# Optimization experiments

Measured on AMD Instinct MI355X. Metric: run time of the kernel, lower is better.

The kernel has to match this reference:

```python
import jax, jax.numpy as jnp
import numpy as np

N, D, H = 50000, 128, 2        # nodes, hidden_size(=ffn_size=out_channels), heads
E = 800000                      # edges
C = D                           # per-head out_channels (PyG TransformerConv)
EPS = 1e-5

def layer_norm(x, g, b):
    mu = jnp.mean(x, axis=-1, keepdims=True)
    var = jnp.mean((x - mu) ** 2, axis=-1, keepdims=True)
    return (x - mu) / jnp.sqrt(var + EPS) * g + b

def setup_inputs() -> dict:
    key = jax.random.key(0)
    ks = jax.random.split(key, 16)
    s_in = 1.0 / np.sqrt(D)
    s_ffn = 1.0 / np.sqrt(D)
    return {
        "x": jax.random.normal(ks[0], (N, D), jnp.float32),
        "edge_index": jax.random.randint(ks[1], (2, E), 0, N, jnp.int64),
        "ln1_g": jnp.ones((D,), jnp.float32),
        "ln1_b": jnp.zeros((D,), jnp.float32),
        "Wq": jax.random.normal(ks[2], (D, H * C), jnp.float32) * s_in,
        "bq": jnp.zeros((H * C,), jnp.float32),
        "Wk": jax.random.normal(ks[3], (D, H * C), jnp.float32) * s_in,
        "bk": jnp.zeros((H * C,), jnp.float32),
        "Wv": jax.random.normal(ks[4], (D, H * C), jnp.float32) * s_in,
        "bv": jnp.zeros((H * C,), jnp.float32),
        "Wskip": jax.random.normal(ks[5], (D, C), jnp.float32) * s_in,
        "bskip": jnp.zeros((C,), jnp.float32),
        "ln2_g": jnp.ones((D,), jnp.float32),
        "ln2_b": jnp.zeros((D,), jnp.float32),
        "W1": jax.random.normal(ks[6], (D, D), jnp.float32) * s_ffn,
        "b1": jnp.zeros((D,), jnp.float32),
        "W2": jax.random.normal(ks[7], (D, D), jnp.float32) * s_ffn,
        "b2": jnp.zeros((D,), jnp.float32),
    }

def reference(x, edge_index, ln1_g, ln1_b, Wq, bq, Wk, bk, Wv, bv,
              Wskip, bskip, ln2_g, ln2_b, W1, b1, W2, b2):
    src, dst = edge_index[0], edge_index[1]  # messages flow src(j) -> dst(i)
    n = x.shape[0]

    # --- self-attention block (pre-norm) ---
    y = layer_norm(x, ln1_g, ln1_b)
    q = (y @ Wq + bq).reshape(n, H, C)
    k = (y @ Wk + bk).reshape(n, H, C)
    v = (y @ Wv + bv).reshape(n, H, C)

    # per-edge attention logits [E, H]
    alpha = jnp.einsum('ehc,ehc->eh', q[dst], k[src]) / jnp.sqrt(jnp.float32(C))
    # softmax over incoming edges of each dst node
    m = jax.ops.segment_max(alpha, dst, num_segments=n)          # [N, H]
    p = jnp.exp(alpha - m[dst])                                  # [E, H]
    denom = jax.ops.segment_sum(p, dst, num_segments=n)          # [N, H]
    a = p / denom[dst]                                           # [E, H]

    attn = jax.ops.segment_sum(a[:, :, None] * v[src], dst, num_segments=n)  # [N,H,C]
    out = attn.mean(axis=1) + (y @ Wskip + bskip)  # concat=False mean + root skip
    x = x + out  # residual (dropout is identity at eval)

    # --- FFN block (pre-norm) ---
    h = layer_norm(x, ln2_g, ln2_b)
    h = jax.nn.gelu(h @ W1 + b1, approximate=False) @ W2 + b2
    return x + h
```

## Files before the change

### kernel.cpp

```cpp
#include <hip/hip_runtime.h>
#include <hip/hip_bf16.h>
#include <math.h>


typedef unsigned short u16;
using short8 = __attribute__((ext_vector_type(8))) short;
using f32x4  = __attribute__((ext_vector_type(4))) float;
using f32x2  = __attribute__((ext_vector_type(2))) float;
using u32x4  = __attribute__((ext_vector_type(4))) unsigned int;

#define EST 64

__device__ __forceinline__ float bf2f(u16 u) {
    return __uint_as_float(((unsigned int)u) << 16);
}
__device__ __forceinline__ u16 f2bf(float f) {
    __hip_bfloat16 h = __float2bfloat16(f);
    return __builtin_bit_cast(u16, h);
}
__device__ __forceinline__ float bfe(short8 v, int j) {
    return bf2f((u16)v[j]);
}
__device__ __forceinline__ void fp8x4_to_f32(int w, float* out) {
    f32x2 lo = __builtin_amdgcn_cvt_pk_f32_fp8(w, false);
    f32x2 hi = __builtin_amdgcn_cvt_pk_f32_fp8(w, true);
    out[0] = lo[0]; out[1] = lo[1]; out[2] = hi[0]; out[3] = hi[1];
}
__device__ __forceinline__ unsigned pack_fp8x4(float4 f) {
    unsigned w = 0;
    w = (unsigned)__builtin_amdgcn_cvt_pk_fp8_f32(f.x, f.y, (int)w, false);
    w = (unsigned)__builtin_amdgcn_cvt_pk_fp8_f32(f.z, f.w, (int)w, true);
    return w;
}

__global__ __launch_bounds__(256) void fused_prep_ln(
    const float* __restrict__ x, const float* __restrict__ ln1g,
    const float* __restrict__ ln1b,
    const float* __restrict__ Wq, const float* __restrict__ Wk,
    const float* __restrict__ Wv, const float* __restrict__ Ws,
    const float* __restrict__ W1, const float* __restrict__ W2,
    const float* __restrict__ bq, const float* __restrict__ bk,
    const float* __restrict__ bv, const float* __restrict__ bs,
    u16* __restrict__ wt, float* __restrict__ bc,
    u16* __restrict__ y, int* __restrict__ cnt, int n,
    const int* __restrict__ edst, const int* __restrict__ esrcIn,
    int* __restrict__ ebuk, int e, int histBlocks)
{
    if (blockIdx.x < (unsigned)histBlocks) {
        int stride = histBlocks * 256;
        for (int i = blockIdx.x * 256 + threadIdx.x; i < e; i += stride) {
            int d = edst[i];
            int r = atomicAdd(&cnt[d], 1);
            if (r < EST) ebuk[(size_t)d * EST + r] = esrcIn[i];
        }
        return;
    }
    int gsz = (gridDim.x - histBlocks) * 256;
    int gtid = (blockIdx.x - histBlocks) * 256 + threadIdx.x;

    for (int i = gtid; i < 147456 + 896; i += gsz) {
        if (i < 147456) {
            const float* W; int N; int base;
            if      (i <  32768) { W = Wq; N = 256; base = 0; }
            else if (i <  65536) { W = Wk; N = 256; base = 32768; }
            else if (i <  98304) { W = Wv; N = 256; base = 65536; }
            else if (i < 114688) { W = Ws; N = 128; base = 98304; }
            else if (i < 131072) { W = W1; N = 128; base = 114688; }
            else                 { W = W2; N = 128; base = 131072; }
            int j = i - base;
            int nIdx = j >> 7, k = j & 127;
            wt[i] = f2bf(W[(size_t)k * N + nIdx]);
        } else {
            int j = i - 147456;
            float v;
            if      (j < 256) v = bq[j];
            else if (j < 512) v = bk[j - 256];
            else if (j < 768) v = bv[j - 512];
            else              v = bs[j - 768];
            bc[j] = v;
        }
    }
    int lane = threadIdx.x & 63;
    int gw = gtid >> 6, nw = gsz >> 6;
    for (int row = gw; row < n; row += nw) {
        size_t base = (size_t)row * 128;
        float v0 = x[base + lane];
        float v1 = x[base + 64 + lane];
        float s1 = v0 + v1, s2 = v0 * v0 + v1 * v1;
        for (int o = 1; o <= 32; o <<= 1) {
            s1 += __shfl_xor(s1, o);
            s2 += __shfl_xor(s2, o);
        }
        float mu = s1 * (1.f / 128.f);
        float var = s2 * (1.f / 128.f) - mu * mu;
        float rstd = rsqrtf(var + 1e-5f);
        y[base + lane]      = f2bf((v0 - mu) * rstd * ln1g[lane] + ln1b[lane]);
        y[base + 64 + lane] = f2bf((v1 - mu) * rstd * ln1g[64 + lane] + ln1b[64 + lane]);
    }
}

__global__ __launch_bounds__(256, 6) void qkv_gemm(
    const u16* __restrict__ A, const u16* __restrict__ Bt,
    const float* __restrict__ bias, u16* __restrict__ qbuf,
    unsigned char* __restrict__ kv,
    float* __restrict__ skip, int n)
{
    __shared__ float epi[4][32 * 33];
    int bid = blockIdx.x;
    int wc = threadIdx.x >> 6, lane = threadIdx.x & 63;
    int r0 = bid * 32;
    int lm = lane & 15, quad = lane >> 4;

    int ar0 = r0 + lm;       if (ar0 > n - 1) ar0 = n - 1;
    int ar1 = r0 + 16 + lm;  if (ar1 > n - 1) ar1 = n - 1;
    const u16* aB0 = A + (size_t)ar0 * 128 + quad * 8;
    const u16* aB1 = A + (size_t)ar1 * 128 + quad * 8;
    short8 a0_0 = *(const short8*)(aB0 + 0);
    short8 a0_1 = *(const short8*)(aB0 + 32);
    short8 a0_2 = *(const short8*)(aB0 + 64);
    short8 a0_3 = *(const short8*)(aB0 + 96);
    short8 a1_0 = *(const short8*)(aB1 + 0);
    short8 a1_1 = *(const short8*)(aB1 + 32);
    short8 a1_2 = *(const short8*)(aB1 + 64);
    short8 a1_3 = *(const short8*)(aB1 + 96);
    asm volatile("" : "+v"(a0_0), "+v"(a0_1), "+v"(a0_2), "+v"(a0_3),
                      "+v"(a1_0), "+v"(a1_1), "+v"(a1_2), "+v"(a1_3));

    int rr = lane & 31, hh = lane >> 5;
    int row = r0 + rr;
    bool rowOk = row < n;
    float* ep = epi[wc];

    for (int by = 0; by < 7; ++by) {
        int c0 = by * 128;
        const u16* bBase = Bt + (size_t)(c0 + wc * 32 + lm) * 128 + quad * 8;
        f32x4 acc[2][2] = {};
#pragma unroll
        for (int kx = 0; kx < 4; ++kx) {
            short8 a0 = (kx == 0) ? a0_0 : (kx == 1) ? a0_1 : (kx == 2) ? a0_2 : a0_3;
            short8 a1 = (kx == 0) ? a1_0 : (kx == 1) ? a1_1 : (kx == 2) ? a1_2 : a1_3;
#pragma unroll
            for (int j = 0; j < 2; ++j) {
                short8 bj = *(const short8*)(bBase + (size_t)j * 16 * 128 + kx * 32);
                acc[0][j] = __builtin_amdgcn_mfma_f32_16x16x32_bf16(a0, bj, acc[0][j], 0, 0, 0);
                acc[1][j] = __builtin_amdgcn_mfma_f32_16x16x32_bf16(a1, bj, acc[1][j], 0, 0, 0);
            }
        }
#pragma unroll
        for (int j = 0; j < 2; ++j) {
            float bv = bias[c0 + wc * 32 + j * 16 + lm];
#pragma unroll
            for (int rt = 0; rt < 2; ++rt)
#pragma unroll
                for (int i2 = 0; i2 < 4; ++i2)
                    ep[(rt * 16 + quad * 4 + i2) * 33 + j * 16 + lm]
                        = acc[rt][j][i2] + bv;
        }
        if (rowOk) {
            const float* ws = ep + rr * 33 + hh * 16;
            int colW = wc * 32 + hh * 16;
            if (c0 < 256) {
                u16* dp = qbuf + (size_t)row * 256 + c0 + colW;
                short8 o0, o1;
#pragma unroll
                for (int jj = 0; jj < 8; ++jj) {
                    o0[jj] = (short)f2bf(ws[jj]);
                    o1[jj] = (short)f2bf(ws[8 + jj]);
                }
                *(short8*)(dp + 0) = o0;
                *(short8*)(dp + 8) = o1;
            } else if (c0 < 512) {
                int kc = (c0 - 256) + colW;
                int h = kc >> 7, c = kc & 127;
                unsigned char* kb = kv + (size_t)row * 512 + h * 256 + (c >> 3) * 16;
                uint2 o0, o1;
                o0.x = pack_fp8x4(make_float4(ws[0],  ws[1],  ws[2],  ws[3]));
                o0.y = pack_fp8x4(make_float4(ws[4],  ws[5],  ws[6],  ws[7]));
                o1.x = pack_fp8x4(make_float4(ws[8],  ws[9],  ws[10], ws[11]));
                o1.y = pack_fp8x4(make_float4(ws[12], ws[13], ws[14], ws[15]));
                *(uint2*)kb = o0;
                *(uint2*)(kb + 16) = o1;
            } else if (c0 < 768) {
                int vc = (c0 - 512) + colW;
                int h = vc >> 7, c = vc & 127;
                unsigned char* vb = kv + (size_t)row * 512 + h * 256 + (c >> 3) * 16 + 8;
                uint2 o0, o1;
                o0.x = pack_fp8x4(make_float4(ws[0],  ws[1],  ws[2],  ws[3]));
                o0.y = pack_fp8x4(make_float4(ws[4],  ws[5],  ws[6],  ws[7]));
                o1.x = pack_fp8x4(make_float4(ws[8],  ws[9],  ws[10], ws[11]));
                o1.y = pack_fp8x4(make_float4(ws[12], ws[13], ws[14], ws[15]));
                *(uint2*)vb = o0;
                *(uint2*)(vb + 16) = o1;
            } else {
                float* dp = skip + (size_t)row * 128 + colW;
#pragma unroll
                for (int m2 = 0; m2 < 4; ++m2)
                    *(float4*)(dp + m2 * 4) = *(const float4*)(ws + m2 * 4);
            }
        }
    }
}

__global__ __launch_bounds__(256) void attn_kernel(
    const u16* __restrict__ qbuf, const unsigned char* __restrict__ kv,
    const int* __restrict__ cnt,
    const int* __restrict__ ebuk, const float* __restrict__ x,
    float* __restrict__ sx, const float* __restrict__ g2,
    const float* __restrict__ b2, u16* __restrict__ y, int n, int nwaves)
{
    int wid = threadIdx.x >> 6, lane = threadIdx.x & 63;
    int gw = blockIdx.x * 4 + wid;
    int slot = lane >> 5;
    int sub  = lane & 15;
    int head = (lane >> 4) & 1;
    int colOff = head * 128 + sub * 8;
    int kvOff  = head * 256 + sub * 16;
    const float scale = 0.08838834764831845f;

    for (int i = gw; i < n; i += nwaves) {
        short8 q8 = *(const short8*)(qbuf + (size_t)i * 256 + colOff);
        float qf[8];
#pragma unroll
        for (int j = 0; j < 8; ++j) qf[j] = bfe(q8, j) * scale;

        int deg = cnt[i]; if (deg > EST) deg = EST;
        int beg = i * EST, end = beg + deg;
        float l = 0.f;
        float acc[8] = {};

        int t = beg + slot;
        for (; t + 14 < end; t += 16) {
            int ss[8];
#pragma unroll
            for (int m = 0; m < 8; ++m) ss[m] = ebuk[t + 2 * m];
            u32x4 k0 = *(const u32x4*)(kv + (size_t)ss[0] * 512 + kvOff);
            u32x4 k1 = *(const u32x4*)(kv + (size_t)ss[1] * 512 + kvOff);
            u32x4 k2 = *(const u32x4*)(kv + (size_t)ss[2] * 512 + kvOff);
            u32x4 k3 = *(const u32x4*)(kv + (size_t)ss[3] * 512 + kvOff);
            u32x4 k4 = *(const u32x4*)(kv + (size_t)ss[4] * 512 + kvOff);
            u32x4 k5 = *(const u32x4*)(kv + (size_t)ss[5] * 512 + kvOff);
            u32x4 k6 = *(const u32x4*)(kv + (size_t)ss[6] * 512 + kvOff);
            u32x4 k7 = *(const u32x4*)(kv + (size_t)ss[7] * 512 + kvOff);
            asm volatile("" : "+v"(k0), "+v"(k1), "+v"(k2), "+v"(k3),
                              "+v"(k4), "+v"(k5), "+v"(k6), "+v"(k7));
            u32x4 kvv[8] = {k0, k1, k2, k3, k4, k5, k6, k7};
            float d[8];
#pragma unroll
            for (int m = 0; m < 8; ++m) {
                float kf[8];
                fp8x4_to_f32((int)kvv[m][0], kf);
                fp8x4_to_f32((int)kvv[m][1], kf + 4);
                float dm = 0.f;
#pragma unroll
                for (int j = 0; j < 8; ++j) dm += qf[j] * kf[j];
                d[m] = dm;
            }
#pragma unroll
            for (int o = 1; o <= 8; o <<= 1)
#pragma unroll
                for (int m = 0; m < 8; ++m) d[m] += __shfl_xor(d[m], o);
            float wv[8];
#pragma unroll
            for (int m = 0; m < 8; ++m) { wv[m] = __expf(d[m]); l += wv[m]; }
#pragma unroll
            for (int m = 0; m < 8; ++m) {
                float vf[8];
                fp8x4_to_f32((int)kvv[m][2], vf);
                fp8x4_to_f32((int)kvv[m][3], vf + 4);
#pragma unroll
                for (int j = 0; j < 8; ++j) acc[j] += wv[m] * vf[j];
            }
        }
        for (; t + 6 < end; t += 8) {
            int s0 = ebuk[t], s1 = ebuk[t + 2], s2 = ebuk[t + 4], s3 = ebuk[t + 6];
            u32x4 kv0 = *(const u32x4*)(kv + (size_t)s0 * 512 + kvOff);
            u32x4 kv1 = *(const u32x4*)(kv + (size_t)s1 * 512 + kvOff);
            u32x4 kv2 = *(const u32x4*)(kv + (size_t)s2 * 512 + kvOff);
            u32x4 kv3 = *(const u32x4*)(kv + (size_t)s3 * 512 + kvOff);
            asm volatile("" : "+v"(kv0), "+v"(kv1), "+v"(kv2), "+v"(kv3));
            float k0f[8], k1f[8], k2f[8], k3f[8];
            float v0f[8], v1f[8], v2f[8], v3f[8];
            fp8x4_to_f32((int)kv0[0], k0f); fp8x4_to_f32((int)kv0[1], k0f + 4);
            fp8x4_to_f32((int)kv1[0], k1f); fp8x4_to_f32((int)kv1[1], k1f + 4);
            fp8x4_to_f32((int)kv2[0], k2f); fp8x4_to_f32((int)kv2[1], k2f + 4);
            fp8x4_to_f32((int)kv3[0], k3f); fp8x4_to_f32((int)kv3[1], k3f + 4);
            fp8x4_to_f32((int)kv0[2], v0f); fp8x4_to_f32((int)kv0[3], v0f + 4);
            fp8x4_to_f32((int)kv1[2], v1f); fp8x4_to_f32((int)kv1[3], v1f + 4);
            fp8x4_to_f32((int)kv2[2], v2f); fp8x4_to_f32((int)kv2[3], v2f + 4);
            fp8x4_to_f32((int)kv3[2], v3f); fp8x4_to_f32((int)kv3[3], v3f + 4);
            float d0 = 0.f, d1 = 0.f, d2 = 0.f, d3 = 0.f;
#pragma unroll
            for (int j = 0; j < 8; ++j) {
                d0 += qf[j] * k0f[j];
                d1 += qf[j] * k1f[j];
                d2 += qf[j] * k2f[j];
                d3 += qf[j] * k3f[j];
            }
#pragma unroll
            for (int o = 1; o <= 8; o <<= 1) {
                d0 += __shfl_xor(d0, o);
                d1 += __shfl_xor(d1, o);
                d2 += __shfl_xor(d2, o);
                d3 += __shfl_xor(d3, o);
            }
            float w0 = __expf(d0), w1 = __expf(d1);
            float w2 = __expf(d2), w3 = __expf(d3);
            l += w0 + w1 + w2 + w3;
#pragma unroll
            for (int j = 0; j < 8; ++j)
                acc[j] += w0 * v0f[j] + w1 * v1f[j] + w2 * v2f[j] + w3 * v3f[j];
        }
        for (; t < end; t += 2) {
            int s0 = ebuk[t];
            u32x4 kv0 = *(const u32x4*)(kv + (size_t)s0 * 512 + kvOff);
            float k0f[8], v0f[8];
            fp8x4_to_f32((int)kv0[0], k0f); fp8x4_to_f32((int)kv0[1], k0f + 4);
            fp8x4_to_f32((int)kv0[2], v0f); fp8x4_to_f32((int)kv0[3], v0f + 4);
            float d0 = 0.f;
#pragma unroll
            for (int j = 0; j < 8; ++j) d0 += qf[j] * k0f[j];
#pragma unroll
            for (int o = 1; o <= 8; o <<= 1) d0 += __shfl_xor(d0, o);
            float w0 = __expf(d0);
            l += w0;
#pragma unroll
            for (int j = 0; j < 8; ++j) acc[j] += w0 * v0f[j];
        }

        float lm2 = l + __shfl_xor(l, 32);
        float inv = (lm2 > 0.f) ? (1.f / lm2) : 0.f;
        float r[8];
#pragma unroll
        for (int j = 0; j < 8; ++j) {
            float a2 = (acc[j] + __shfl_xor(acc[j], 32)) * inv;
            r[j] = 0.5f * (a2 + __shfl_xor(a2, 16));
        }

        if (lane < 16) {
            size_t base = (size_t)i * 128 + sub * 8;
            float4 xv0 = *(const float4*)(x + base);
            float4 xv1 = *(const float4*)(x + base + 4);
            float4 sk0 = *(const float4*)(sx + base);
            float4 sk1 = *(const float4*)(sx + base + 4);
            r[0] += xv0.x + sk0.x; r[1] += xv0.y + sk0.y;
            r[2] += xv0.z + sk0.z; r[3] += xv0.w + sk0.w;
            r[4] += xv1.x + sk1.x; r[5] += xv1.y + sk1.y;
            r[6] += xv1.z + sk1.z; r[7] += xv1.w + sk1.w;
            *(float4*)(sx + base)     = make_float4(r[0], r[1], r[2], r[3]);
            *(float4*)(sx + base + 4) = make_float4(r[4], r[5], r[6], r[7]);
            float s1 = 0.f, s2 = 0.f;
#pragma unroll
            for (int j = 0; j < 8; ++j) { s1 += r[j]; s2 += r[j] * r[j]; }
#pragma unroll
            for (int o = 1; o <= 8; o <<= 1) {
                s1 += __shfl_xor(s1, o);
                s2 += __shfl_xor(s2, o);
            }
            float mu = s1 * (1.f / 128.f);
            float var = s2 * (1.f / 128.f) - mu * mu;
            float rstd = rsqrtf(var + 1e-5f);
            short8 o8;
#pragma unroll
            for (int j = 0; j < 8; ++j)
                o8[j] = (short)f2bf((r[j] - mu) * rstd * g2[sub * 8 + j] + b2[sub * 8 + j]);
            *(short8*)(y + base) = o8;
        }
    }
}

__global__ __launch_bounds__(256) void ffn_kernel(
    const u16* __restrict__ y2, const u16* __restrict__ W1T,
    const float* __restrict__ b1, const u16* __restrict__ W2T,
    const float* __restrict__ b2, const float* __restrict__ x2,
    float* __restrict__ out, int n)
{
    __shared__ u16 t1[64 * 136];
    int wid = threadIdx.x >> 6, lane = threadIdx.x & 63;
    int lm = lane & 15, quad = lane >> 4;
    int r0 = blockIdx.x * 64 + wid * 16;

    const u16* aBase = y2 + (size_t)(r0 + lm) * 128 + quad * 8;
    f32x4 acc[8] = {};
#pragma unroll
    for (int kk = 0; kk < 128; kk += 32) {
        short8 a0 = *(const short8*)(aBase + kk);
#pragma unroll
        for (int j = 0; j < 8; ++j) {
            short8 bj = *(const short8*)(W1T + (size_t)(j * 16 + lm) * 128 + quad * 8 + kk);
            acc[j] = __builtin_amdgcn_mfma_f32_16x16x32_bf16(a0, bj, acc[j], 0, 0, 0);
        }
    }
#pragma unroll
    for (int j = 0; j < 8; ++j) {
        int col = j * 16 + lm;
        float bv = b1[col];
#pragma unroll
        for (int i2 = 0; i2 < 4; ++i2) {
            int rl = wid * 16 + quad * 4 + i2;
            float v = acc[j][i2] + bv;
            v = 0.5f * v * (1.f + erff(v * 0.70710678118654752f));
            t1[rl * 136 + col] = f2bf(v);
        }
    }

    f32x4 acc2[8] = {};
#pragma unroll
    for (int kk = 0; kk < 128; kk += 32) {
        short8 a0 = *(const short8*)(t1 + (wid * 16 + lm) * 136 + quad * 8 + kk);
#pragma unroll
        for (int j = 0; j < 8; ++j) {
            short8 bj = *(const short8*)(W2T + (size_t)(j * 16 + lm) * 128 + quad * 8 + kk);
            acc2[j] = __builtin_amdgcn_mfma_f32_16x16x32_bf16(a0, bj, acc2[j], 0, 0, 0);
        }
    }
#pragma unroll
    for (int j = 0; j < 8; ++j) {
        int col = j * 16 + lm;
        float bv = b2[col];
#pragma unroll
        for (int i2 = 0; i2 < 4; ++i2) {
            int row = r0 + quad * 4 + i2;
            if (row >= n) continue;
            size_t ob = (size_t)row * 128 + col;
            out[ob] = acc2[j][i2] + bv + x2[ob];
        }
    }
}

extern "C" void kernel_launch(void* const* d_in, const int* in_sizes, int n_in,
                              void* d_out, int out_size, void* d_ws, size_t ws_size,
                              hipStream_t stream)
{
    const float* x    = (const float*)d_in[0];
    const int*   ei   = (const int*)d_in[1];

    int n = in_sizes[0] / 128;
    int e = in_sizes[1] / 2;
    const int* src  = ei;
    const int* dstp = ei + e;

    char* w = (char*)d_ws;
    size_t off = 0;
    auto alloc = [&](size_t bytes) -> void* {
        void* p = w + off;
        off = (off + bytes + 255) & ~(size_t)255;
        return p;
    };
    u16*   y    = (u16*)alloc((size_t)n * 128 * 2);
    u16*   qbuf = (u16*)alloc((size_t)n * 256 * 2);
    unsigned char* kvb = (unsigned char*)alloc((size_t)n * 512);
    float* sx   = (float*)alloc((size_t)n * 128 * 4);
    u16*   wt   = (u16*)alloc((size_t)147456 * 2);
    float* bc   = (float*)alloc(896 * 4);
    int* cnt    = (int*)alloc((size_t)n * 4);
    int* ebuk   = (int*)alloc((size_t)n * EST * 4);

    int gr   = (n + 63) / 64;
    int gr32 = (n + 31) / 32;
    int histBlocks = 512;
    int attnBlocks = 2048;

    hipMemsetAsync(cnt, 0, (size_t)n * sizeof(int), stream);
    fused_prep_ln<<<2048 + histBlocks, 256, 0, stream>>>(
        x, (const float*)d_in[2], (const float*)d_in[3],
        (const float*)d_in[4], (const float*)d_in[6], (const float*)d_in[8],
        (const float*)d_in[10], (const float*)d_in[14], (const float*)d_in[16],
        (const float*)d_in[5], (const float*)d_in[7], (const float*)d_in[9],
        (const float*)d_in[11], wt, bc, y, cnt, n, dstp, src, ebuk, e, histBlocks);
    qkv_gemm<<<gr32, 256, 0, stream>>>(y, wt, bc, qbuf, kvb, sx, n);
    attn_kernel<<<attnBlocks, 256, 0, stream>>>(qbuf, kvb, cnt, ebuk, x, sx,
                                                (const float*)d_in[12],
                                                (const float*)d_in[13], y, n,
                                                attnBlocks * 4);
    ffn_kernel<<<gr, 256, 0, stream>>>(y, wt + 114688, (const float*)d_in[15],
                                       wt + 131072, (const float*)d_in[17],
                                       sx, (float*)d_out, n);
}
```

Measured before the change: 349.0 us.

## Retile FFN kernel to 32-row blocks with column-split waves sharing LDS intermediate

The FFN kernel now processes 32 rows per block. Each of the four waves computes a 32-column slice for both row tiles, instead of one wave owning 16 full rows. The GELU intermediate is shared through LDS with a block barrier, A fragments are preloaded into registers, launch bounds ask for higher occupancy, and the grid doubles. The histogram block count in the prep kernel is also doubled. This cuts per-wave accumulator registers and W reads per wave, at the cost of a __syncthreads and more blocks.

```diff
diff --git a/kernel.cpp b/kernel.cpp
--- a/kernel.cpp
+++ b/kernel.cpp
@@ -368,62 +368,101 @@
     }
 }
 
-__global__ __launch_bounds__(256) void ffn_kernel(
+__global__ __launch_bounds__(256, 6) void ffn_kernel(
     const u16* __restrict__ y2, const u16* __restrict__ W1T,
     const float* __restrict__ b1, const u16* __restrict__ W2T,
     const float* __restrict__ b2, const float* __restrict__ x2,
     float* __restrict__ out, int n)
 {
-    __shared__ u16 t1[64 * 136];
-    int wid = threadIdx.x >> 6, lane = threadIdx.x & 63;
+    __shared__ u16 t1[32][136];
+    int wc = threadIdx.x >> 6, lane = threadIdx.x & 63;
     int lm = lane & 15, quad = lane >> 4;
-    int r0 = blockIdx.x * 64 + wid * 16;
-
-    const u16* aBase = y2 + (size_t)(r0 + lm) * 128 + quad * 8;
-    f32x4 acc[8] = {};
-#pragma unroll
-    for (int kk = 0; kk < 128; kk += 32) {
-        short8 a0 = *(const short8*)(aBase + kk);
-#pragma unroll
-        for (int j = 0; j < 8; ++j) {
-            short8 bj = *(const short8*)(W1T + (size_t)(j * 16 + lm) * 128 + quad * 8 + kk);
-            acc[j] = __builtin_amdgcn_mfma_f32_16x16x32_bf16(a0, bj, acc[j], 0, 0, 0);
-        }
-    }
-#pragma unroll
-    for (int j = 0; j < 8; ++j) {
-        int col = j * 16 + lm;
+    int r0 = blockIdx.x * 32;
+
+    int ar0 = r0 + lm;       if (ar0 > n - 1) ar0 = n - 1;
+    int ar1 = r0 + 16 + lm;  if (ar1 > n - 1) ar1 = n - 1;
+    const u16* aB0 = y2 + (size_t)ar0 * 128 + quad * 8;
+    const u16* aB1 = y2 + (size_t)ar1 * 128 + quad * 8;
+    short8 a0_0 = *(const short8*)(aB0 + 0);
+    short8 a0_1 = *(const short8*)(aB0 + 32);
+    short8 a0_2 = *(const short8*)(aB0 + 64);
+    short8 a0_3 = *(const short8*)(aB0 + 96);
+    short8 a1_0 = *(const short8*)(aB1 + 0);
+    short8 a1_1 = *(const short8*)(aB1 + 32);
+    short8 a1_2 = *(const short8*)(aB1 + 64);
+    short8 a1_3 = *(const short8*)(aB1 + 96);
+    asm volatile("" : "+v"(a0_0), "+v"(a0_1), "+v"(a0_2), "+v"(a0_3),
+                      "+v"(a1_0), "+v"(a1_1), "+v"(a1_2), "+v"(a1_3));
+
+    f32x4 acc[2][2] = {};
+    {
+        const u16* bBase = W1T + (size_t)(wc * 32 + lm) * 128 + quad * 8;
+#pragma unroll
+        for (int kx = 0; kx < 4; ++kx) {
+            short8 a0 = (kx == 0) ? a0_0 : (kx == 1) ? a0_1 : (kx == 2) ? a0_2 : a0_3;
+            short8 a1 = (kx == 0) ? a1_0 : (kx == 1) ? a1_1 : (kx == 2) ? a1_2 : a1_3;
+#pragma unroll
+            for (int j = 0; j < 2; ++j) {
+                short8 bj = *(const short8*)(bBase + (size_t)j * 16 * 128 + kx * 32);
+                acc[0][j] = __builtin_amdgcn_mfma_f32_16x16x32_bf16(a0, bj, acc[0][j], 0, 0, 0);
+                acc[1][j] = __builtin_amdgcn_mfma_f32_16x16x32_bf16(a1, bj, acc[1][j], 0, 0, 0);
+            }
+        }
+    }
+#pragma unroll
+    for (int j = 0; j < 2; ++j) {
+        int col = wc * 32 + j * 16 + lm;
         float bv = b1[col];
 #pragma unroll
-        for (int i2 = 0; i2 < 4; ++i2) {
-            int rl = wid * 16 + quad * 4 + i2;
-            float v = acc[j][i2] + bv;
-            v = 0.5f * v * (1.f + erff(v * 0.70710678118654752f));
-            t1[rl * 136 + col] = f2bf(v);
-        }
-    }
-
-    f32x4 acc2[8] = {};
-#pragma unroll
-    for (int kk = 0; kk < 128; kk += 32) {
-        short8 a0 = *(const short8*)(t1 + (wid * 16 + lm) * 136 + quad * 8 + kk);
-#pragma unroll
-        for (int j = 0; j < 8; ++j) {
-            short8 bj = *(const short8*)(W2T + (size_t)(j * 16 + lm) * 128 + quad * 8 + kk);
-            acc2[j] = __builtin_amdgcn_mfma_f32_16x16x32_bf16(a0, bj, acc2[j], 0, 0, 0);
-        }
-    }
-#pragma unroll
-    for (int j = 0; j < 8; ++j) {
-        int col = j * 16 + lm;
+        for (int rt = 0; rt < 2; ++rt)
+#pragma unroll
+            for (int i2 = 0; i2 < 4; ++i2) {
+                float v = acc[rt][j][i2] + bv;
+                v = 0.5f * v * (1.f + erff(v * 0.70710678118654752f));
+                t1[rt * 16 + quad * 4 + i2][col] = f2bf(v);
+            }
+    }
+    __syncthreads();
+
+    short8 c0_0 = *(const short8*)&t1[lm]     [quad * 8 + 0];
+    short8 c0_1 = *(const short8*)&t1[lm]     [quad * 8 + 32];
+    short8 c0_2 = *(const short8*)&t1[lm]     [quad * 8 + 64];
+    short8 c0_3 = *(const short8*)&t1[lm]     [quad * 8 + 96];
+    short8 c1_0 = *(const short8*)&t1[16 + lm][quad * 8 + 0];
+    short8 c1_1 = *(const short8*)&t1[16 + lm][quad * 8 + 32];
+    short8 c1_2 = *(const short8*)&t1[16 + lm][quad * 8 + 64];
+    short8 c1_3 = *(const short8*)&t1[16 + lm][quad * 8 + 96];
+    asm volatile("" : "+v"(c0_0), "+v"(c0_1), "+v"(c0_2), "+v"(c0_3),
+                      "+v"(c1_0), "+v"(c1_1), "+v"(c1_2), "+v"(c1_3));
+
+    f32x4 acc2[2][2] = {};
+    {
+        const u16* bBase = W2T + (size_t)(wc * 32 + lm) * 128 + quad * 8;
+#pragma unroll
+        for (int kx = 0; kx < 4; ++kx) {
+            short8 a0 = (kx == 0) ? c0_0 : (kx == 1) ? c0_1 : (kx == 2) ? c0_2 : c0_3;
+            short8 a1 = (kx == 0) ? c1_0 : (kx == 1) ? c1_1 : (kx == 2) ? c1_2 : c1_3;
+#pragma unroll
+            for (int j = 0; j < 2; ++j) {
+                short8 bj = *(const short8*)(bBase + (size_t)j * 16 * 128 + kx * 32);
+                acc2[0][j] = __builtin_amdgcn_mfma_f32_16x16x32_bf16(a0, bj, acc2[0][j], 0, 0, 0);
+                acc2[1][j] = __builtin_amdgcn_mfma_f32_16x16x32_bf16(a1, bj, acc2[1][j], 0, 0, 0);
+            }
+        }
+    }
+#pragma unroll
+    for (int j = 0; j < 2; ++j) {
+        int col = wc * 32 + j * 16 + lm;
         float bv = b2[col];
 #pragma unroll
-        for (int i2 = 0; i2 < 4; ++i2) {
-            int row = r0 + quad * 4 + i2;
-            if (row >= n) continue;
-            size_t ob = (size_t)row * 128 + col;
-            out[ob] = acc2[j][i2] + bv + x2[ob];
-        }
+        for (int rt = 0; rt < 2; ++rt)
+#pragma unroll
+            for (int i2 = 0; i2 < 4; ++i2) {
+                int row = r0 + rt * 16 + quad * 4 + i2;
+                if (row >= n) continue;
+                size_t ob = (size_t)row * 128 + col;
+                out[ob] = acc2[rt][j][i2] + bv + x2[ob];
+            }
     }
 }
 
@@ -455,9 +494,8 @@
     int* cnt    = (int*)alloc((size_t)n * 4);
     int* ebuk   = (int*)alloc((size_t)n * EST * 4);
 
-    int gr   = (n + 63) / 64;
     int gr32 = (n + 31) / 32;
-    int histBlocks = 512;
+    int histBlocks = 1024;
     int attnBlocks = 2048;
 
     hipMemsetAsync(cnt, 0, (size_t)n * sizeof(int), stream);
@@ -472,7 +510,7 @@
                                                 (const float*)d_in[12],
                                                 (const float*)d_in[13], y, n,
                                                 attnBlocks * 4);
-    ffn_kernel<<<gr, 256, 0, stream>>>(y, wt + 114688, (const float*)d_in[15],
-                                       wt + 131072, (const float*)d_in[17],
-                                       sx, (float*)d_out, n);
-}
+    ffn_kernel<<<gr32, 256, 0, stream>>>(y, wt + 114688, (const float*)d_in[15],
+                                         wt + 131072, (const float*)d_in[17],
+                                         sx, (float*)d_out, n);
+}
```

After: 346.6 us. Within noise of the previous version (-0.7%).
